# Performance work log

Hardware: AMD Instinct MI355X
Metric: run time of the kernel (lower is better)

The kernel has to match this reference:

```python
import jax, jax.numpy as jnp
import numpy as np
from jax import lax

# FEMBATinyFullInput config
B = 16; H = 22; W_IN = 20480
PH, PW = 2, 16; SH, SW = 2, 16
EMBED = 35
GH = (H - PH) // SH + 1            # 11
GW = (W_IN - PW) // SW + 1         # 1280
L = GW; DM = GH * EMBED            # seq_len=1280, d_model=385
DI = 256; N = 4; K = 4             # d_inner (capped), d_state, conv_kernel
DT_R = 25                          # ceil(d_model/16), Mamba dt_rank
NB = 2; NC = 2


def fq(x):
    """8-bit symmetric fake-quant (QuantIdentity) with straight-through estimator."""
    s = jnp.maximum(jnp.max(jnp.abs(x)), 1e-8) / 127.0
    q = jnp.clip(jnp.round(x / s), -128, 127) * s
    return x + lax.stop_gradient(q - x)


def layernorm(x, g, b, eps=1e-5):
    m = jnp.mean(x, -1, keepdims=True)
    v = jnp.var(x, -1, keepdims=True)
    return (x - m) * lax.rsqrt(v + eps) * g + b


def selective_scan(xc, dt, A, Bc, Cc):
    # xc, dt: [B,L,DI]; A: [DI,N]; Bc, Cc: [B,L,N]
    dA = jnp.exp(dt[..., None] * A)                              # [B,L,DI,N]
    dBx = dt[..., None] * Bc[:, :, None, :] * xc[..., None]      # [B,L,DI,N]

    def step(h, inp):
        dA_t, dBx_t, C_t = inp
        h = dA_t * h + dBx_t
        return h, jnp.einsum('bdn,bn->bd', h, C_t)

    h0 = jnp.zeros((xc.shape[0], DI, N), xc.dtype)
    _, ys = lax.scan(step, h0, (dA.transpose(1, 0, 2, 3),
                                dBx.transpose(1, 0, 2, 3),
                                Cc.transpose(1, 0, 2)))
    return ys.transpose(1, 0, 2)                                 # [B,L,DI]


def mamba_dir(x, p):
    in_w, cw, cb, xp_w, dt_w, dt_b, A_log, Dp, out_w = p
    xz = x @ in_w                                                # [B,L,2*DI]
    xs, z = jnp.split(xz, 2, axis=-1)
    # depthwise causal conv1d over time
    xt = lax.conv_general_dilated(xs.transpose(0, 2, 1), cw[:, None, :],
                                  (1,), [(K - 1, 0)],
                                  feature_group_count=DI,
                                  dimension_numbers=('NCH', 'OIH', 'NCH'))
    xc = jax.nn.silu(xt.transpose(0, 2, 1) + cb)                 # [B,L,DI]
    proj = xc @ xp_w                                             # [B,L,DT_R+2N]
    dtr, Bc, Cc = jnp.split(proj, [DT_R, DT_R + N], axis=-1)
    dt = jax.nn.softplus(dtr @ dt_w + dt_b)                      # [B,L,DI]
    A = -jnp.exp(A_log)
    y = selective_scan(xc, dt, A, Bc, Cc) + Dp * xc
    y = y * jax.nn.silu(z)
    return y @ out_w                                             # [B,L,DM]


def mamba_bidir(x, p):
    # bidirectional_strategy='add': forward pass + flipped pass, summed
    fwd = mamba_dir(x, p)
    bwd = jnp.flip(mamba_dir(jnp.flip(x, 1), p), 1)
    return fq(fwd + bwd)


def _forward(x, pe_w, pe_b, pos_embed, in_w, conv_w, conv_b, xp_w, dt_w,
             dt_b, A_log, Dp, out_w, ln_g, ln_b, cls_w, cls_b):
    x = fq(x)                                                    # input_quant
    # QuantPatchEmbed: int8 weight conv2d, kernel=stride=(2,16)
    x = lax.conv_general_dilated(x, fq(pe_w), (SH, SW), 'VALID',
                                 dimension_numbers=('NCHW', 'OIHW', 'NCHW'))
    x = x + pe_b[None, :, None, None]                            # [B,EMBED,GH,GW]
    x = x.transpose(0, 3, 2, 1).reshape(x.shape[0], L, DM)       # [B,L,DM]
    x = fq(x)
    pos = fq(fq(pos_embed))                                      # pos_quant + scale_equalizer
    x = fq(fq(x) + pos)                                          # scale_equalizer chain
    for i in range(NB):
        p = (in_w[i], conv_w[i], conv_b[i], xp_w[i], dt_w[i], dt_b[i],
             A_log[i], Dp[i], out_w[i])
        x = fq(layernorm(x + mamba_bidir(x, p), ln_g[i], ln_b[i]))
    x = jnp.mean(x, axis=1)                                      # AdaptiveAvgPool1d(1)
    x = fq(x)                                                    # pre_classifier_quant
    return x @ fq(cls_w) + cls_b                                 # QuantLinear


def setup_inputs() -> dict:
    key = jax.random.key(0)
    ks = jax.random.split(key, 10)
    rn = lambda k, shape, s: (jax.random.normal(k, shape) * s).astype(jnp.float32)
    dt_init = float(np.log(np.expm1(0.01)))
    return {
        'x': jax.random.normal(ks[0], (B, 1, H, W_IN), jnp.float32),
        'pe_w': rn(ks[1], (EMBED, 1, PH, PW), 0.1),
        'pe_b': jnp.zeros((EMBED,), jnp.float32),
        'pos_embed': rn(ks[2], (1, L, DM), 0.02),
        'in_w': rn(ks[3], (NB, DM, 2 * DI), 0.05),
        'conv_w': rn(ks[4], (NB, DI, K), 0.1),
        'conv_b': jnp.zeros((NB, DI), jnp.float32),
        'xp_w': rn(ks[5], (NB, DI, DT_R + 2 * N), 0.05),
        'dt_w': rn(ks[6], (NB, DT_R, DI), 0.1),
        'dt_b': jnp.full((NB, DI), dt_init, jnp.float32),
        'A_log': jnp.log(jnp.tile(jnp.arange(1, N + 1, dtype=jnp.float32), (NB, DI, 1))),
        'Dp': jnp.ones((NB, DI), jnp.float32),
        'out_w': rn(ks[7], (NB, DI, DM), 0.05),
        'ln_g': jnp.ones((NB, DM), jnp.float32),
        'ln_b': jnp.zeros((NB, DM), jnp.float32),
        'cls_w': rn(ks[8], (DM, NC), 0.05),
        'cls_b': jnp.zeros((NC,), jnp.float32),
    }


def reference(x, pe_w, pe_b, pos_embed, in_w, conv_w, conv_b, xp_w, dt_w,
              dt_b, A_log, Dp, out_w, ln_g, ln_b, cls_w, cls_b):
    return _forward(x, pe_w, pe_b, pos_embed, in_w, conv_w, conv_b, xp_w,
                    dt_w, dt_b, A_log, Dp, out_w, ln_g, ln_b, cls_w, cls_b)
```

## Files before the change

### kernel.cpp

```cpp
#include <hip/hip_runtime.h>
#include <hip/hip_bf16.h>
#include <math.h>

#define B_    16
#define H_    22
#define W_    20480
#define EMB   35
#define GH_   11
#define GW_   1280
#define L_    1280
#define DM_   385
#define DI_   256
#define N_    4
#define K_    4
#define DTR_  25
#define ROWS_ (B_*L_)
#define NX_   ((long)ROWS_*DM_)
#define LDM_  ((long)L_*DM_)
#define CH_   64
#define CHL_  20
#define KPI_  800
#define KPA_  400
#define KPO_  768
#define WAO_  512

#define NSLOT 8
#define SSTR  16
#define SCALW 128

typedef __attribute__((ext_vector_type(8))) short short8;
typedef __attribute__((ext_vector_type(4))) float f32x4;
typedef unsigned short ushort;

__device__ __forceinline__ void atomicMaxF(float* a, float v) {
  atomicMax(reinterpret_cast<int*>(a), __float_as_int(v));
}

__device__ __forceinline__ float fq_scale(const float* pmax) {
  float m = pmax[0];
  #pragma unroll
  for (int i = 1; i < NSLOT; i++) m = fmaxf(m, pmax[i * SSTR]);
  return fmaxf(m, 1e-8f) / 127.f;
}
__device__ __forceinline__ float fq_apply(float x, float s) {
  float r = rintf(x / s);
  r = fminf(fmaxf(r, -128.f), 127.f);
  return r * s;
}

__device__ __forceinline__ ushort f2bf(float f) {
  union { float f; unsigned u; } v; v.f = f;
  unsigned r = v.u + 0x7FFF + ((v.u >> 16) & 1);
  return (ushort)(r >> 16);
}
__device__ __forceinline__ float bf2f(ushort h) {
  union { unsigned u; float f; } v; v.u = ((unsigned)h) << 16;
  return v.f;
}

__device__ __forceinline__ void blockAtomicMax(float v, float* out, float* sm) {
  #pragma unroll
  for (int o = 32; o > 0; o >>= 1) v = fmaxf(v, __shfl_down(v, o));
  if ((threadIdx.x & 63) == 0) sm[threadIdx.x >> 6] = v;
  __syncthreads();
  if (threadIdx.x == 0) {
    int nw = (blockDim.x + 63) >> 6;
    for (int i = 1; i < nw; i++) v = fmaxf(v, sm[i]);
    int slot = (blockIdx.x + blockIdx.y * 4 + blockIdx.z) & (NSLOT - 1);
    atomicMaxF(out + slot * SSTR, v);
  }
}

__global__ void k_zero(float* s) { s[blockIdx.x * 256 + threadIdx.x] = 0.f; }

__global__ void k_absmax(const float* __restrict__ src, long n, float* __restrict__ out) {
  __shared__ float smr[8];
  float m = 0.f;
  for (long i = (long)blockIdx.x * blockDim.x + threadIdx.x; i < n;
       i += (long)gridDim.x * blockDim.x)
    m = fmaxf(m, fabsf(src[i]));
  blockAtomicMax(m, out, smr);
}

__global__ void k_fq4(const float4* __restrict__ src, float4* __restrict__ dst, long n4,
                      const float* __restrict__ pmax, float* __restrict__ nextmax,
                      ushort* __restrict__ a2) {
  __shared__ float smr[8];
  float s = fq_scale(pmax);
  float m = 0.f;
  for (long i = (long)blockIdx.x * blockDim.x + threadIdx.x; i < n4;
       i += (long)gridDim.x * blockDim.x) {
    float4 v = src[i];
    float r0 = fminf(fmaxf(rintf(v.x / s), -128.f), 127.f);
    float r1 = fminf(fmaxf(rintf(v.y / s), -128.f), 127.f);
    float r2 = fminf(fmaxf(rintf(v.z / s), -128.f), 127.f);
    float r3 = fminf(fmaxf(rintf(v.w / s), -128.f), 127.f);
    float4 q = make_float4(r0 * s, r1 * s, r2 * s, r3 * s);
    dst[i] = q;
    m = fmaxf(m, fmaxf(fmaxf(fabsf(q.x), fabsf(q.y)), fmaxf(fabsf(q.z), fabsf(q.w))));
    if (a2) {
      long ii = i * 4;
      long mm = ii / 385; int kk = (int)(ii - mm * 385);
      float rr[4] = {r0, r1, r2, r3};
      #pragma unroll
      for (int j = 0; j < 4; j++) {
        a2[mm * KPA_ + kk] = f2bf(rr[j]);
        if (++kk == 385) { kk = 0; mm++; }
      }
    }
  }
  if (nextmax) blockAtomicMax(m, nextmax, smr);
}

__global__ void k_addpos4(float4* __restrict__ x, const float4* __restrict__ p2,
                          const float* __restrict__ pmax, float* __restrict__ nextmax) {
  __shared__ float smr[8];
  float s = fq_scale(pmax);
  float m = 0.f;
  const long n4 = NX_ / 4, l4 = LDM_ / 4;
  for (long i = (long)blockIdx.x * blockDim.x + threadIdx.x; i < n4;
       i += (long)gridDim.x * blockDim.x) {
    float4 v = x[i];
    float4 p = p2[i % l4];
    float4 o;
    o.x = fq_apply(v.x, s) + p.x;
    o.y = fq_apply(v.y, s) + p.y;
    o.z = fq_apply(v.z, s) + p.z;
    o.w = fq_apply(v.w, s) + p.w;
    x[i] = o;
    m = fmaxf(m, fmaxf(fmaxf(fabsf(o.x), fabsf(o.y)), fmaxf(fabsf(o.z), fabsf(o.w))));
  }
  blockAtomicMax(m, nextmax, smr);
}

__global__ __launch_bounds__(320) void k_patchfq(const float* __restrict__ x,
                                                 const float* __restrict__ pew,
                                                 const float* __restrict__ peb,
                                                 const float* __restrict__ sx_,
                                                 const float* __restrict__ sw_,
                                                 float* __restrict__ out,
                                                 float* __restrict__ nextmax) {
  __shared__ float xs[2][64][20];
  __shared__ float smr[8];
  int tid = threadIdx.x;
  int gwt = blockIdx.x, gh = blockIdx.y, b = blockIdx.z;
  float sx = fq_scale(sx_), sw = fq_scale(sw_);
  if (tid < 256) {
    int gwl = tid >> 2, pw = (tid & 3) * 4;
    #pragma unroll
    for (int ph = 0; ph < 2; ph++) {
      const float* src = x + ((long)b * H_ + gh * 2 + ph) * W_ + (long)gwt * 1024 + tid * 4;
      float4 v = *reinterpret_cast<const float4*>(src);
      xs[ph][gwl][pw + 0] = fq_apply(v.x, sx);
      xs[ph][gwl][pw + 1] = fq_apply(v.y, sx);
      xs[ph][gwl][pw + 2] = fq_apply(v.z, sx);
      xs[ph][gwl][pw + 3] = fq_apply(v.w, sx);
    }
  }
  __syncthreads();
  float mx = 0.f;
  if (tid < 280) {
    int e = tid % 35;
    int g0 = (tid / 35) * 8;
    float w[32];
    #pragma unroll
    for (int j = 0; j < 32; j++) w[j] = fq_apply(pew[e * 32 + j], sw);
    float bias = peb[e];
    long obase = ((long)b * GW_ + (long)gwt * 64) * DM_ + gh * 35 + e;
    #pragma unroll
    for (int gi = 0; gi < 8; gi++) {
      int gw = g0 + gi;
      float acc = bias;
      #pragma unroll
      for (int pw = 0; pw < 16; pw++) {
        acc = fmaf(xs[0][gw][pw], w[pw], acc);
        acc = fmaf(xs[1][gw][pw], w[16 + pw], acc);
      }
      out[obase + (long)gw * DM_] = acc;
      mx = fmaxf(mx, fabsf(acc));
    }
  }
  blockAtomicMax(mx, nextmax, smr);
}

__global__ void k_wsplit(const float* __restrict__ W, ushort* __restrict__ out,
                         int K, int N, int Kw, int Kp, long total, int terms) {
  long idx = (long)blockIdx.x * 256 + threadIdx.x;
  if (idx >= total) return;
  int k = (int)(idx % Kp);
  int n = (int)(idx / Kp);
  int t = k / Kw, kk = k - t * Kw;
  ushort r = 0;
  if (n < N && kk < K) {
    float w = W[(long)kk * N + n];
    ushort hi = f2bf(w);
    r = (t == terms - 1) ? f2bf(w - bf2f(hi)) : hi;
  }
  out[idx] = r;
}

__global__ void k_asplit2(const float* __restrict__ Y, ushort* __restrict__ A2) {
  long idx = (long)blockIdx.x * 256 + threadIdx.x;
  long m = idx >> 9; int k = (int)(idx & 511);
  int t = k >> 8, kk = k & 255;
  float v = Y[m * DI_ + kk] + Y[(m + ROWS_) * DI_ + kk];
  ushort hi = f2bf(v);
  A2[idx] = t ? f2bf(v - bf2f(hi)) : hi;
}

__global__ void k_padzero(ushort* __restrict__ A2) {
  long idx = (long)blockIdx.x * 256 + threadIdx.x;
  long m = idx / 15; int c = (int)(idx - m * 15);
  A2[m * KPA_ + 385 + c] = 0;
}

template<bool AMAX>
__global__ __launch_bounds__(256) void k_mgemm(const ushort* __restrict__ A2,
                                               const ushort* __restrict__ W2T,
                                               float* __restrict__ C,
                                               int Nreal, int Kp, int Wa,
                                               const float* __restrict__ sptr,
                                               float* __restrict__ amax_out) {
  __shared__ ushort Alds[4][128][8];
  __shared__ ushort Blds[4][128][8];
  __shared__ float smr[8];
  int tid = threadIdx.x;
  int lane = tid & 63, wave = tid >> 6;
  int wm = wave >> 1, wn = wave & 1;
  int m0 = blockIdx.y * 128, n0 = blockIdx.x * 128;
  f32x4 acc[4][4];
  #pragma unroll
  for (int i = 0; i < 4; i++)
    #pragma unroll
    for (int j = 0; j < 4; j++) acc[i][j] = (f32x4){0.f, 0.f, 0.f, 0.f};

  for (int k0 = 0; k0 < Kp; k0 += 32) {
    #pragma unroll
    for (int r = 0; r < 2; r++) {
      int id = tid + r * 256;
      int row = id >> 2, sl = id & 3;
      int kc = k0 + sl * 8; if (kc >= Wa) kc -= Wa;
      short8 va = *reinterpret_cast<const short8*>(A2 + (long)(m0 + row) * Wa + kc);
      *reinterpret_cast<short8*>(&Alds[sl][row][0]) = va;
      short8 vb = *reinterpret_cast<const short8*>(W2T + (long)(n0 + row) * Kp + k0 + sl * 8);
      *reinterpret_cast<short8*>(&Blds[sl][row][0]) = vb;
    }
    __syncthreads();
    int sl = lane >> 4, rr = lane & 15;
    short8 af[4], bf4[4];
    #pragma unroll
    for (int i = 0; i < 4; i++)
      af[i] = *reinterpret_cast<const short8*>(&Alds[sl][wm * 64 + i * 16 + rr][0]);
    #pragma unroll
    for (int j = 0; j < 4; j++)
      bf4[j] = *reinterpret_cast<const short8*>(&Blds[sl][wn * 64 + j * 16 + rr][0]);
    #pragma unroll
    for (int i = 0; i < 4; i++)
      #pragma unroll
      for (int j = 0; j < 4; j++)
        acc[i][j] = __builtin_amdgcn_mfma_f32_16x16x32_bf16(af[i], bf4[j], acc[i][j], 0, 0, 0);
    __syncthreads();
  }

  float s = sptr ? fq_scale(sptr) : 1.0f;
  float mx = 0.f;
  int cfr = lane & 15, rbase = (lane >> 4) * 4;
  #pragma unroll
  for (int i = 0; i < 4; i++) {
    int gmb = m0 + wm * 64 + i * 16 + rbase;
    #pragma unroll
    for (int j = 0; j < 4; j++) {
      int gn = n0 + wn * 64 + j * 16 + cfr;
      if (gn < Nreal) {
        #pragma unroll
        for (int rg = 0; rg < 4; rg++) {
          float v = acc[i][j][rg] * s;
          C[(long)(gmb + rg) * Nreal + gn] = v;
          mx = fmaxf(mx, fabsf(v));
        }
      }
    }
  }
  if (AMAX) blockAtomicMax(mx, amax_out, smr);
}

template<bool AMAX>
__global__ __launch_bounds__(256) void k_gemm(const float* __restrict__ A,
                                              const float* __restrict__ W,
                                              float* __restrict__ C,
                                              int M, int N, int Kd,
                                              float* __restrict__ amax_out) {
  __shared__ __align__(16) float As[16][68];
  __shared__ __align__(16) float Bs[16][68];
  __shared__ float smr[8];
  int tx = threadIdx.x & 15, ty = threadIdx.x >> 4;
  int m0 = blockIdx.y * 64, n0 = blockIdx.x * 64;
  float acc[4][4] = {};
  for (int k0 = 0; k0 < Kd; k0 += 16) {
    #pragma unroll
    for (int r = 0; r < 4; r++) {
      int id = threadIdx.x + r * 256;
      int mm = id >> 4, kk = id & 15;
      int gm = m0 + mm, gk = k0 + kk;
      As[kk][mm] = (gm < M && gk < Kd) ? A[(long)gm * Kd + gk] : 0.f;
    }
    #pragma unroll
    for (int r = 0; r < 4; r++) {
      int id = threadIdx.x + r * 256;
      int kk = id >> 6, nn = id & 63;
      int gk = k0 + kk, gn = n0 + nn;
      Bs[kk][nn] = (gk < Kd && gn < N) ? W[(long)gk * N + gn] : 0.f;
    }
    __syncthreads();
    #pragma unroll
    for (int kk = 0; kk < 16; kk++) {
      float4 a4 = *reinterpret_cast<const float4*>(&As[kk][ty * 4]);
      float4 b4 = *reinterpret_cast<const float4*>(&Bs[kk][tx * 4]);
      float av[4] = {a4.x, a4.y, a4.z, a4.w};
      float bv[4] = {b4.x, b4.y, b4.z, b4.w};
      #pragma unroll
      for (int i = 0; i < 4; i++)
        #pragma unroll
        for (int j = 0; j < 4; j++)
          acc[i][j] = fmaf(av[i], bv[j], acc[i][j]);
    }
    __syncthreads();
  }
  float mx = 0.f;
  #pragma unroll
  for (int i = 0; i < 4; i++) {
    int gm = m0 + ty * 4 + i;
    if (gm < M) {
      #pragma unroll
      for (int j = 0; j < 4; j++) {
        int gn = n0 + tx * 4 + j;
        if (gn < N) {
          C[(long)gm * N + gn] = acc[i][j];
          mx = fmaxf(mx, fabsf(acc[i][j]));
        }
      }
    }
  }
  if (AMAX) blockAtomicMax(mx, amax_out, smr);
}

__global__ __launch_bounds__(256) void k_conv2(const float* __restrict__ xz,
                                               const float* __restrict__ cw,
                                               const float* __restrict__ cb,
                                               float* __restrict__ xcout) {
  int d = threadIdx.x;
  int t0 = blockIdx.x * 16, b = blockIdx.y;
  long base = (long)b * L_;
  float w0 = cw[d * 4 + 0], w1 = cw[d * 4 + 1];
  float w2 = cw[d * 4 + 2], w3 = cw[d * 4 + 3];
  float bias = cb[d];
  float win[22];
  #pragma unroll
  for (int i = 0; i < 22; i++) {
    int t = t0 - 3 + i;
    win[i] = (t >= 0 && t < L_) ? xz[(base + t) * (2 * DI_) + d] : 0.f;
  }
  #pragma unroll
  for (int i = 0; i < 16; i++) {
    int t = t0 + i;
    float a0 = bias;
    a0 = fmaf(w0, win[i + 0], a0);
    a0 = fmaf(w1, win[i + 1], a0);
    a0 = fmaf(w2, win[i + 2], a0);
    a0 = fmaf(w3, win[i + 3], a0);
    float a1 = bias;
    a1 = fmaf(w0, win[i + 6], a1);
    a1 = fmaf(w1, win[i + 5], a1);
    a1 = fmaf(w2, win[i + 4], a1);
    a1 = fmaf(w3, win[i + 3], a1);
    float s0 = 1.f / (1.f + expf(-a0));
    float s1 = 1.f / (1.f + expf(-a1));
    long o = (base + t) * DI_ + d;
    xcout[o] = a0 * s0;
    xcout[(long)ROWS_ * DI_ + o] = a1 * s1;
  }
}

__device__ __forceinline__ float softplusf(float x) {
  return fmaxf(x, 0.f) + log1pf(expf(-fabsf(x)));
}

__global__ __launch_bounds__(256) void k_dtp(const float* __restrict__ proj,
                                             const float* __restrict__ dtw,
                                             const float* __restrict__ dtb,
                                             float* __restrict__ dty) {
  __shared__ float pr[16][26];
  int d = threadIdx.x;
  long g0 = (long)blockIdx.x * 16;
  for (int i = threadIdx.x; i < 16 * DTR_; i += 256) {
    int r = i / DTR_, j = i - r * DTR_;
    pr[r][j] = proj[(g0 + r) * 33 + j];
  }
  float dwr[DTR_];
  #pragma unroll
  for (int r = 0; r < DTR_; r++) dwr[r] = dtw[r * DI_ + d];
  float dbv = dtb[d];
  __syncthreads();
  #pragma unroll
  for (int r = 0; r < 16; r++) {
    float acc = dbv;
    #pragma unroll
    for (int j = 0; j < DTR_; j++) acc = fmaf(pr[r][j], dwr[j], acc);
    dty[(g0 + r) * DI_ + d] = softplusf(acc);
  }
}

__global__ __launch_bounds__(256) void k_scan1(const float* __restrict__ xc,
                                               const float* __restrict__ proj,
                                               const float* __restrict__ A_log,
                                               const float* __restrict__ dty,
                                               float* __restrict__ Hend,
                                               float* __restrict__ Pend) {
  int b = blockIdx.y, c = blockIdx.x, d = threadIdx.x, dir = blockIdx.z;
  float A[4];
  #pragma unroll
  for (int n = 0; n < 4; n++) A[n] = -expf(A_log[d * 4 + n]);
  long base = (long)b * L_;
  int step0 = c * CHL_;
  long row0 = base + (dir ? (L_ - 1 - step0) : step0);
  long doff = (long)dir * ROWS_;
  int rs = dir ? -1 : 1;
  long dstr = (long)rs * DI_;
  const float* pdt = dty + (doff + row0) * DI_ + d;
  const float* pxc = xc + (doff + row0) * DI_ + d;
  const float* pp  = proj + (doff + row0) * 33;
  float h[4] = {0.f, 0.f, 0.f, 0.f};
  float P[4] = {1.f, 1.f, 1.f, 1.f};
  for (int s = 0; s < CHL_; s++) {
    float dtv = *pdt;
    float xcv = *pxc;
    float dx = dtv * xcv;
    #pragma unroll
    for (int n = 0; n < 4; n++) {
      float dA = expf(dtv * A[n]);
      h[n] = dA * h[n] + dx * pp[DTR_ + n];
      P[n] *= dA;
    }
    pdt += dstr; pxc += dstr; pp += rs * 33;
  }
  long o = (((long)dir * B_ + b) * CH_ + c) * 1024 + d * 4;
  *reinterpret_cast<float4*>(Hend + o) = make_float4(h[0], h[1], h[2], h[3]);
  *reinterpret_cast<float4*>(Pend + o) = make_float4(P[0], P[1], P[2], P[3]);
}

__global__ __launch_bounds__(256) void k_carry(const float* __restrict__ Hend,
                                               const float* __restrict__ Pend,
                                               float* __restrict__ Carry) {
  int tid = blockIdx.x * 256 + threadIdx.x;
  int be = tid >> 10, i = tid & 1023;
  float carry = 0.f;
  for (int c = 0; c < CH_; c++) {
    long o = ((long)be * CH_ + c) * 1024 + i;
    Carry[o] = carry;
    carry = Pend[o] * carry + Hend[o];
  }
}

__global__ __launch_bounds__(256) void k_scan2(const float* __restrict__ xc,
                                               const float* __restrict__ proj,
                                               const float* __restrict__ A_log,
                                               const float* __restrict__ Dp,
                                               const float* __restrict__ xz,
                                               const float* __restrict__ Carry,
                                               float* dty) {
  int b = blockIdx.y, c = blockIdx.x, d = threadIdx.x, dir = blockIdx.z;
  float A[4];
  #pragma unroll
  for (int n = 0; n < 4; n++) A[n] = -expf(A_log[d * 4 + n]);
  long base = (long)b * L_;
  int step0 = c * CHL_;
  long row0 = base + (dir ? (L_ - 1 - step0) : step0);
  long doff = (long)dir * ROWS_;
  int rs = dir ? -1 : 1;
  long dstr = (long)rs * DI_;
  float* pdy = dty + (doff + row0) * DI_ + d;
  const float* pxc = xc + (doff + row0) * DI_ + d;
  const float* pz  = xz + row0 * (2 * DI_) + DI_ + d;
  const float* pp  = proj + (doff + row0) * 33;
  long o = (((long)dir * B_ + b) * CH_ + c) * 1024 + d * 4;
  float4 cv = *reinterpret_cast<const float4*>(Carry + o);
  float h[4] = {cv.x, cv.y, cv.z, cv.w};
  float Dv = Dp[d];
  for (int s = 0; s < CHL_; s++) {
    float dtv = *pdy;
    float xcv = *pxc;
    float zv  = *pz;
    float dx = dtv * xcv;
    float acc = 0.f;
    #pragma unroll
    for (int n = 0; n < 4; n++) {
      float dA = expf(dtv * A[n]);
      h[n] = dA * h[n] + dx * pp[DTR_ + n];
      acc = fmaf(h[n], pp[DTR_ + N_ + n], acc);
    }
    float yv = fmaf(Dv, xcv, acc);
    float sig = 1.f / (1.f + expf(-zv));
    yv *= zv * sig;
    *pdy = yv;
    pdy += dstr; pxc += dstr; pz += rs * (2 * DI_); pp += rs * 33;
  }
}

__global__ __launch_bounds__(256) void k_ln(const float* __restrict__ x2,
                                            float* __restrict__ mo,
                                            const float* __restrict__ smo,
                                            const float* __restrict__ g,
                                            const float* __restrict__ bta,
                                            float* __restrict__ nextmax) {
  __shared__ float smr[4];
  int lane = threadIdx.x & 63;
  int wid = blockIdx.x * 4 + (threadIdx.x >> 6);
  float s = fq_scale(smo);
  float wmax = 0.f;
  for (int row = wid; row < ROWS_; row += 2560) {
    const float* xr = x2 + (long)row * DM_;
    float* mr = mo + (long)row * DM_;
    float v[7];
    float lsum = 0.f;
    #pragma unroll
    for (int k = 0; k < 6; k++) {
      int c = lane + k * 64;
      v[k] = xr[c] + fq_apply(mr[c], s);
      lsum += v[k];
    }
    v[6] = 0.f;
    if (lane == 0) v[6] = xr[384] + fq_apply(mr[384], s);
    lsum += v[6];
    #pragma unroll
    for (int o = 32; o > 0; o >>= 1) lsum += __shfl_xor(lsum, o);
    float mean = lsum / 385.f;
    float lvar = 0.f;
    #pragma unroll
    for (int k = 0; k < 6; k++) { float dd = v[k] - mean; lvar += dd * dd; }
    if (lane == 0) { float dd = v[6] - mean; lvar += dd * dd; }
    #pragma unroll
    for (int o = 32; o > 0; o >>= 1) lvar += __shfl_xor(lvar, o);
    float rs = 1.f / sqrtf(lvar / 385.f + 1e-5f);
    #pragma unroll
    for (int k = 0; k < 6; k++) {
      int c = lane + k * 64;
      float o2 = (v[k] - mean) * rs * g[c] + bta[c];
      mr[c] = o2;
      wmax = fmaxf(wmax, fabsf(o2));
    }
    if (lane == 0) {
      float o2 = (v[6] - mean) * rs * g[384] + bta[384];
      mr[384] = o2;
      wmax = fmaxf(wmax, fabsf(o2));
    }
  }
  blockAtomicMax(wmax, nextmax, smr);
}

__global__ __launch_bounds__(256) void k_pool1(const float* __restrict__ x2,
                                               float* __restrict__ part) {
  int b = blockIdx.x, ch = blockIdx.y, tid = threadIdx.x;
  float s0 = 0.f, s1 = 0.f;
  for (int l = ch * 64; l < ch * 64 + 64; l++) {
    const float* row = x2 + ((long)b * L_ + l) * DM_;
    s0 += row[tid];
    if (tid < DM_ - 256) s1 += row[tid + 256];
  }
  long o = ((long)b * 20 + ch) * DM_;
  part[o + tid] = s0;
  if (tid < DM_ - 256) part[o + tid + 256] = s1;
}

__global__ void k_pool2(const float* __restrict__ part, float* __restrict__ pool,
                        float* __restrict__ nextmax) {
  __shared__ float smr[8];
  int idx = blockIdx.x * 256 + threadIdx.x;
  float mv = 0.f;
  if (idx < B_ * DM_) {
    int b = idx / DM_, c = idx % DM_;
    float s = 0.f;
    for (int ch = 0; ch < 20; ch++) s += part[((long)b * 20 + ch) * DM_ + c];
    float mean = s / (float)L_;
    pool[idx] = mean;
    mv = fabsf(mean);
  }
  blockAtomicMax(mv, nextmax, smr);
}

__global__ __launch_bounds__(128) void k_cls(const float* __restrict__ pool,
                                             const float* __restrict__ clsw,
                                             const float* __restrict__ clsb,
                                             const float* __restrict__ sp_,
                                             const float* __restrict__ sw_,
                                             float* __restrict__ out) {
  __shared__ float smr[2];
  int b = blockIdx.x >> 1, c = blockIdx.x & 1;
  float sp = fq_scale(sp_), sw = fq_scale(sw_);
  float acc = 0.f;
  for (int k = threadIdx.x; k < DM_; k += 128) {
    float xv = fq_apply(pool[b * DM_ + k], sp);
    float wv = fq_apply(clsw[k * 2 + c], sw);
    acc = fmaf(xv, wv, acc);
  }
  #pragma unroll
  for (int o = 32; o > 0; o >>= 1) acc += __shfl_down(acc, o);
  if ((threadIdx.x & 63) == 0) smr[threadIdx.x >> 6] = acc;
  __syncthreads();
  if (threadIdx.x == 0) out[blockIdx.x] = smr[0] + smr[1] + clsb[c];
}

extern "C" void kernel_launch(void* const* d_in, const int* in_sizes, int n_in,
                              void* d_out, int out_size, void* d_ws, size_t ws_size,
                              hipStream_t stream) {
  const float* x    = (const float*)d_in[0];
  const float* pew  = (const float*)d_in[1];
  const float* peb  = (const float*)d_in[2];
  const float* pos  = (const float*)d_in[3];
  const float* in_w = (const float*)d_in[4];
  const float* cw   = (const float*)d_in[5];
  const float* cb   = (const float*)d_in[6];
  const float* xpw  = (const float*)d_in[7];
  const float* dtw  = (const float*)d_in[8];
  const float* dtb  = (const float*)d_in[9];
  const float* alog = (const float*)d_in[10];
  const float* dp   = (const float*)d_in[11];
  const float* outw = (const float*)d_in[12];
  const float* lng  = (const float*)d_in[13];
  const float* lnb  = (const float*)d_in[14];
  const float* clsw = (const float*)d_in[15];
  const float* clsb = (const float*)d_in[16];

  float* ws    = (float*)d_ws;
  float* SCAL  = ws;
  float* P2    = ws + 2048;
  float* X2    = P2 + LDM_;
  float* XZ    = X2 + NX_;
  float* XC    = XZ + (long)ROWS_ * 512;
  float* PROJ  = XC + 2L * ROWS_ * DI_;
  float* Y     = PROJ + 2L * ROWS_ * 33;
  float* MO    = Y + 2L * ROWS_ * DI_;
  float* POOL  = MO + NX_;
  float* PART  = POOL + 8192;
  float* A2IN_f= PART + 131072;
  float* W2I_f = A2IN_f + 4096000;
  float* W2O_f = W2I_f + 409600;
  float*  HEND = MO;
  float*  PEND = MO + 2097152;
  float*  CARR = MO + 4194304;
  ushort* A2Y  = (ushort*)XZ;
  ushort* A2IN = (ushort*)A2IN_f;
  ushort* W2TI = (ushort*)W2I_f;
  ushort* W2TO = (ushort*)W2O_f;

  #define SC(i) (SCAL + (i) * SCALW)

  k_zero<<<8, 256, 0, stream>>>(SCAL);

  for (int blk = 0; blk < 2; blk++) {
    k_wsplit<<<1600, 256, 0, stream>>>(in_w + (long)blk * DM_ * 512,
                                       W2TI + (long)blk * 512 * KPI_,
                                       DM_, 512, KPA_, KPI_, 512L * KPI_, 2);
    k_wsplit<<<1536, 256, 0, stream>>>(outw + (long)blk * DI_ * DM_,
                                       W2TO + (long)blk * 512 * KPO_,
                                       DI_, DM_, 256, KPO_, 512L * KPO_, 3);
  }
  k_padzero<<<1200, 256, 0, stream>>>(A2IN);

  k_absmax<<<2048, 256, 0, stream>>>(x, (long)B_ * H_ * W_, SC(0));
  k_absmax<<<8, 256, 0, stream>>>(pew, EMB * 2 * 16, SC(1));
  k_absmax<<<512, 256, 0, stream>>>(pos, LDM_, SC(4));
  k_patchfq<<<dim3(20, 11, 16), 320, 0, stream>>>(x, pew, peb, SC(0), SC(1), X2, SC(2));

  k_fq4<<<512, 256, 0, stream>>>((const float4*)pos, (float4*)P2, LDM_ / 4,
                                 SC(4), nullptr, nullptr);

  k_addpos4<<<2048, 256, 0, stream>>>((float4*)X2, (const float4*)P2, SC(2), SC(6));
  k_fq4<<<2048, 256, 0, stream>>>((const float4*)X2, (float4*)X2, NX_ / 4,
                                  SC(6), nullptr, A2IN);

  const float* in_scale[2] = {SC(6), SC(8)};
  for (int blk = 0; blk < 2; blk++) {
    k_mgemm<false><<<dim3(4, 160), 256, 0, stream>>>(
        A2IN, W2TI + (long)blk * 512 * KPI_, XZ, 512, KPI_, KPA_, in_scale[blk], nullptr);
    k_conv2<<<dim3(80, 16), 256, 0, stream>>>(XZ, cw + blk * DI_ * K_,
                                              cb + blk * DI_, XC);
    k_gemm<false><<<dim3(1, 640), 256, 0, stream>>>(
        XC, xpw + (long)blk * DI_ * 33, PROJ, 2 * ROWS_, 33, DI_, nullptr);
    k_dtp<<<2560, 256, 0, stream>>>(PROJ, dtw + blk * DTR_ * DI_, dtb + blk * DI_, Y);
    k_scan1<<<dim3(CH_, B_, 2), 256, 0, stream>>>(XC, PROJ, alog + blk * DI_ * N_,
                                                  Y, HEND, PEND);
    k_carry<<<128, 256, 0, stream>>>(HEND, PEND, CARR);
    k_scan2<<<dim3(CH_, B_, 2), 256, 0, stream>>>(XC, PROJ, alog + blk * DI_ * N_,
                                                  dp + blk * DI_, XZ, CARR, Y);
    k_asplit2<<<40960, 256, 0, stream>>>(Y, A2Y);
    k_mgemm<true><<<dim3(4, 160), 256, 0, stream>>>(
        A2Y, W2TO + (long)blk * 512 * KPO_, MO, DM_, KPO_, WAO_, nullptr, SC(7 + blk * 2));
    k_ln<<<640, 256, 0, stream>>>(X2, MO, SC(7 + blk * 2),
                                  lng + blk * DM_, lnb + blk * DM_, SC(8 + blk * 2));
    k_fq4<<<2048, 256, 0, stream>>>((const float4*)MO, (float4*)X2, NX_ / 4,
                                    SC(8 + blk * 2), nullptr,
                                    blk == 0 ? A2IN : nullptr);
  }

  k_pool1<<<dim3(16, 20), 256, 0, stream>>>(X2, PART);
  k_pool2<<<25, 256, 0, stream>>>(PART, POOL, SC(11));
  k_absmax<<<4, 256, 0, stream>>>(clsw, DM_ * 2, SC(12));
  k_cls<<<32, 128, 0, stream>>>(POOL, clsw, clsb, SC(11), SC(12), (float*)d_out);
}
```

Before: 697.2 us.

## Route x_proj GEMM through split-bf16 MFMA kernel with hi/lo conv output

The depthwise conv now writes its SiLU output as a hi/lo bf16 pair (split-precision) in a 512-wide row layout, not as fp32. The x_proj GEMM then runs on the existing bf16 matrix-core kernel with a pre-split weight, replacing the scalar fp32 tiled GEMM. The scan kernels read and sum the hi/lo pair to rebuild xc. Risks are a small precision change, N=33 padded to a 128-column tile wasting MFMA work, and an extra weight-split launch.

```diff
diff --git a/kernel.cpp b/kernel.cpp
--- a/kernel.cpp
+++ b/kernel.cpp
@@ -284,70 +284,10 @@
   if (AMAX) blockAtomicMax(mx, amax_out, smr);
 }
 
-template<bool AMAX>
-__global__ __launch_bounds__(256) void k_gemm(const float* __restrict__ A,
-                                              const float* __restrict__ W,
-                                              float* __restrict__ C,
-                                              int M, int N, int Kd,
-                                              float* __restrict__ amax_out) {
-  __shared__ __align__(16) float As[16][68];
-  __shared__ __align__(16) float Bs[16][68];
-  __shared__ float smr[8];
-  int tx = threadIdx.x & 15, ty = threadIdx.x >> 4;
-  int m0 = blockIdx.y * 64, n0 = blockIdx.x * 64;
-  float acc[4][4] = {};
-  for (int k0 = 0; k0 < Kd; k0 += 16) {
-    #pragma unroll
-    for (int r = 0; r < 4; r++) {
-      int id = threadIdx.x + r * 256;
-      int mm = id >> 4, kk = id & 15;
-      int gm = m0 + mm, gk = k0 + kk;
-      As[kk][mm] = (gm < M && gk < Kd) ? A[(long)gm * Kd + gk] : 0.f;
-    }
-    #pragma unroll
-    for (int r = 0; r < 4; r++) {
-      int id = threadIdx.x + r * 256;
-      int kk = id >> 6, nn = id & 63;
-      int gk = k0 + kk, gn = n0 + nn;
-      Bs[kk][nn] = (gk < Kd && gn < N) ? W[(long)gk * N + gn] : 0.f;
-    }
-    __syncthreads();
-    #pragma unroll
-    for (int kk = 0; kk < 16; kk++) {
-      float4 a4 = *reinterpret_cast<const float4*>(&As[kk][ty * 4]);
-      float4 b4 = *reinterpret_cast<const float4*>(&Bs[kk][tx * 4]);
-      float av[4] = {a4.x, a4.y, a4.z, a4.w};
-      float bv[4] = {b4.x, b4.y, b4.z, b4.w};
-      #pragma unroll
-      for (int i = 0; i < 4; i++)
-        #pragma unroll
-        for (int j = 0; j < 4; j++)
-          acc[i][j] = fmaf(av[i], bv[j], acc[i][j]);
-    }
-    __syncthreads();
-  }
-  float mx = 0.f;
-  #pragma unroll
-  for (int i = 0; i < 4; i++) {
-    int gm = m0 + ty * 4 + i;
-    if (gm < M) {
-      #pragma unroll
-      for (int j = 0; j < 4; j++) {
-        int gn = n0 + tx * 4 + j;
-        if (gn < N) {
-          C[(long)gm * N + gn] = acc[i][j];
-          mx = fmaxf(mx, fabsf(acc[i][j]));
-        }
-      }
-    }
-  }
-  if (AMAX) blockAtomicMax(mx, amax_out, smr);
-}
-
 __global__ __launch_bounds__(256) void k_conv2(const float* __restrict__ xz,
                                                const float* __restrict__ cw,
                                                const float* __restrict__ cb,
-                                               float* __restrict__ xcout) {
+                                               ushort* __restrict__ xch) {
   int d = threadIdx.x;
   int t0 = blockIdx.x * 16, b = blockIdx.y;
   long base = (long)b * L_;
@@ -373,11 +313,15 @@
     a1 = fmaf(w1, win[i + 5], a1);
     a1 = fmaf(w2, win[i + 4], a1);
     a1 = fmaf(w3, win[i + 3], a1);
-    float s0 = 1.f / (1.f + expf(-a0));
-    float s1 = 1.f / (1.f + expf(-a1));
-    long o = (base + t) * DI_ + d;
-    xcout[o] = a0 * s0;
-    xcout[(long)ROWS_ * DI_ + o] = a1 * s1;
+    float v0 = a0 * (1.f / (1.f + expf(-a0)));
+    float v1 = a1 * (1.f / (1.f + expf(-a1)));
+    long g0o = (base + t) * 512 + d;
+    ushort h0 = f2bf(v0), h1 = f2bf(v1);
+    xch[g0o] = h0;
+    xch[g0o + 256] = f2bf(v0 - bf2f(h0));
+    long g1o = ((long)ROWS_ + base + t) * 512 + d;
+    xch[g1o] = h1;
+    xch[g1o + 256] = f2bf(v1 - bf2f(h1));
   }
 }
 
@@ -410,7 +354,7 @@
   }
 }
 
-__global__ __launch_bounds__(256) void k_scan1(const float* __restrict__ xc,
+__global__ __launch_bounds__(256) void k_scan1(const ushort* __restrict__ xch,
                                                const float* __restrict__ proj,
                                                const float* __restrict__ A_log,
                                                const float* __restrict__ dty,
@@ -425,15 +369,14 @@
   long row0 = base + (dir ? (L_ - 1 - step0) : step0);
   long doff = (long)dir * ROWS_;
   int rs = dir ? -1 : 1;
-  long dstr = (long)rs * DI_;
   const float* pdt = dty + (doff + row0) * DI_ + d;
-  const float* pxc = xc + (doff + row0) * DI_ + d;
+  const ushort* pxc = xch + (doff + row0) * 512 + d;
   const float* pp  = proj + (doff + row0) * 33;
   float h[4] = {0.f, 0.f, 0.f, 0.f};
   float P[4] = {1.f, 1.f, 1.f, 1.f};
   for (int s = 0; s < CHL_; s++) {
     float dtv = *pdt;
-    float xcv = *pxc;
+    float xcv = bf2f(pxc[0]) + bf2f(pxc[256]);
     float dx = dtv * xcv;
     #pragma unroll
     for (int n = 0; n < 4; n++) {
@@ -441,7 +384,7 @@
       h[n] = dA * h[n] + dx * pp[DTR_ + n];
       P[n] *= dA;
     }
-    pdt += dstr; pxc += dstr; pp += rs * 33;
+    pdt += (long)rs * DI_; pxc += (long)rs * 512; pp += rs * 33;
   }
   long o = (((long)dir * B_ + b) * CH_ + c) * 1024 + d * 4;
   *reinterpret_cast<float4*>(Hend + o) = make_float4(h[0], h[1], h[2], h[3]);
@@ -461,7 +404,7 @@
   }
 }
 
-__global__ __launch_bounds__(256) void k_scan2(const float* __restrict__ xc,
+__global__ __launch_bounds__(256) void k_scan2(const ushort* __restrict__ xch,
                                                const float* __restrict__ proj,
                                                const float* __restrict__ A_log,
                                                const float* __restrict__ Dp,
@@ -477,9 +420,8 @@
   long row0 = base + (dir ? (L_ - 1 - step0) : step0);
   long doff = (long)dir * ROWS_;
   int rs = dir ? -1 : 1;
-  long dstr = (long)rs * DI_;
   float* pdy = dty + (doff + row0) * DI_ + d;
-  const float* pxc = xc + (doff + row0) * DI_ + d;
+  const ushort* pxc = xch + (doff + row0) * 512 + d;
   const float* pz  = xz + row0 * (2 * DI_) + DI_ + d;
   const float* pp  = proj + (doff + row0) * 33;
   long o = (((long)dir * B_ + b) * CH_ + c) * 1024 + d * 4;
@@ -488,7 +430,7 @@
   float Dv = Dp[d];
   for (int s = 0; s < CHL_; s++) {
     float dtv = *pdy;
-    float xcv = *pxc;
+    float xcv = bf2f(pxc[0]) + bf2f(pxc[256]);
     float zv  = *pz;
     float dx = dtv * xcv;
     float acc = 0.f;
@@ -502,7 +444,8 @@
     float sig = 1.f / (1.f + expf(-zv));
     yv *= zv * sig;
     *pdy = yv;
-    pdy += dstr; pxc += dstr; pz += rs * (2 * DI_); pp += rs * 33;
+    pdy += (long)rs * DI_; pxc += (long)rs * 512;
+    pz += rs * (2 * DI_); pp += rs * 33;
   }
 }
 
@@ -635,8 +578,8 @@
   float* P2    = ws + 2048;
   float* X2    = P2 + LDM_;
   float* XZ    = X2 + NX_;
-  float* XC    = XZ + (long)ROWS_ * 512;
-  float* PROJ  = XC + 2L * ROWS_ * DI_;
+  float* XCH_f = XZ + (long)ROWS_ * 512;
+  float* PROJ  = XCH_f + 2L * ROWS_ * DI_;
   float* Y     = PROJ + 2L * ROWS_ * 33;
   float* MO    = Y + 2L * ROWS_ * DI_;
   float* POOL  = MO + NX_;
@@ -644,13 +587,16 @@
   float* A2IN_f= PART + 131072;
   float* W2I_f = A2IN_f + 4096000;
   float* W2O_f = W2I_f + 409600;
+  float* W2X_f = W2O_f + 393216;
   float*  HEND = MO;
   float*  PEND = MO + 2097152;
   float*  CARR = MO + 4194304;
   ushort* A2Y  = (ushort*)XZ;
+  ushort* XCH  = (ushort*)XCH_f;
   ushort* A2IN = (ushort*)A2IN_f;
   ushort* W2TI = (ushort*)W2I_f;
   ushort* W2TO = (ushort*)W2O_f;
+  ushort* W2TX = (ushort*)W2X_f;
 
   #define SC(i) (SCAL + (i) * SCALW)
 
@@ -663,6 +609,9 @@
     k_wsplit<<<1536, 256, 0, stream>>>(outw + (long)blk * DI_ * DM_,
                                        W2TO + (long)blk * 512 * KPO_,
                                        DI_, DM_, 256, KPO_, 512L * KPO_, 3);
+    k_wsplit<<<384, 256, 0, stream>>>(xpw + (long)blk * DI_ * 33,
+                                      W2TX + (long)blk * 128 * KPO_,
+                                      DI_, 33, 256, KPO_, 128L * KPO_, 3);
   }
   k_padzero<<<1200, 256, 0, stream>>>(A2IN);
 
@@ -683,14 +632,14 @@
     k_mgemm<false><<<dim3(4, 160), 256, 0, stream>>>(
         A2IN, W2TI + (long)blk * 512 * KPI_, XZ, 512, KPI_, KPA_, in_scale[blk], nullptr);
     k_conv2<<<dim3(80, 16), 256, 0, stream>>>(XZ, cw + blk * DI_ * K_,
-                                              cb + blk * DI_, XC);
-    k_gemm<false><<<dim3(1, 640), 256, 0, stream>>>(
-        XC, xpw + (long)blk * DI_ * 33, PROJ, 2 * ROWS_, 33, DI_, nullptr);
+                                              cb + blk * DI_, XCH);
+    k_mgemm<false><<<dim3(1, 320), 256, 0, stream>>>(
+        XCH, W2TX + (long)blk * 128 * KPO_, PROJ, 33, KPO_, WAO_, nullptr, nullptr);
     k_dtp<<<2560, 256, 0, stream>>>(PROJ, dtw + blk * DTR_ * DI_, dtb + blk * DI_, Y);
-    k_scan1<<<dim3(CH_, B_, 2), 256, 0, stream>>>(XC, PROJ, alog + blk * DI_ * N_,
+    k_scan1<<<dim3(CH_, B_, 2), 256, 0, stream>>>(XCH, PROJ, alog + blk * DI_ * N_,
                                                   Y, HEND, PEND);
     k_carry<<<128, 256, 0, stream>>>(HEND, PEND, CARR);
-    k_scan2<<<dim3(CH_, B_, 2), 256, 0, stream>>>(XC, PROJ, alog + blk * DI_ * N_,
+    k_scan2<<<dim3(CH_, B_, 2), 256, 0, stream>>>(XCH, PROJ, alog + blk * DI_ * N_,
                                                   dp + blk * DI_, XZ, CARR, Y);
     k_asplit2<<<40960, 256, 0, stream>>>(Y, A2Y);
     k_mgemm<true><<<dim3(4, 160), 256, 0, stream>>>(
```

Result: faster. 675.4 us (-3.1%).
